# Optimization experiments

Hardware: AMD Instinct MI355X
Metric: run time of the kernel (lower is better)

The kernel has to match this reference:

```python
import jax, jax.numpy as jnp
import numpy as np

B, T, S = 4, 2048, 512
HID, ND, NH = 2048, 1024, 16
HD = HID // NH  # 128
GATING_INIT = -4.0


def setup_inputs() -> dict:
    key = jax.random.key(0)
    ks = jax.random.split(key, 12)
    sc_h = 1.0 / np.sqrt(HID)
    sc_n = 1.0 / np.sqrt(ND)
    mask = jax.random.bernoulli(ks[2], 0.9, (B, S))
    mask = mask.at[:, 0].set(True)  # avoid fully-masked rows (NaN softmax)
    return {
        "hidden_states": jax.random.normal(ks[0], (B, T, HID), jnp.float32),
        "notes": jax.random.normal(ks[1], (B, S, ND), jnp.float32),
        "notes_mask": mask,
        "q_w": jax.random.normal(ks[3], (HID, HID), jnp.float32) * sc_h,
        "q_b": jax.random.normal(ks[4], (HID,), jnp.float32) * 0.01,
        "k_w": jax.random.normal(ks[5], (HID, ND), jnp.float32) * sc_n,
        "k_b": jax.random.normal(ks[6], (HID,), jnp.float32) * 0.01,
        "v_w": jax.random.normal(ks[7], (HID, ND), jnp.float32) * sc_n,
        "v_b": jax.random.normal(ks[8], (HID,), jnp.float32) * 0.01,
        "o_w": jax.random.normal(ks[9], (HID, HID), jnp.float32) * sc_h,
        "o_b": jax.random.normal(ks[10], (HID,), jnp.float32) * 0.01,
        "gate": jnp.full((1,), GATING_INIT, jnp.float32),
    }


def reference(hidden_states, notes, notes_mask, q_w, q_b, k_w, k_b, v_w, v_b, o_w, o_b, gate):
    # projections (torch Linear: x @ W^T + b)
    q = hidden_states @ q_w.T + q_b            # (B,T,HID)
    k = notes @ k_w.T + k_b                    # (B,S,HID)
    v = notes @ v_w.T + v_b                    # (B,S,HID)
    q = q.reshape(B, T, NH, HD).transpose(0, 2, 1, 3)  # (B,H,T,D)
    k = k.reshape(B, S, NH, HD).transpose(0, 2, 1, 3)  # (B,H,S,D)
    v = v.reshape(B, S, NH, HD).transpose(0, 2, 1, 3)
    scores = jnp.einsum("bhtd,bhsd->bhts", q, k) / jnp.sqrt(jnp.float32(HD))
    scores = jnp.where(notes_mask[:, None, None, :], scores, -jnp.inf)
    attn = jax.nn.softmax(scores, axis=-1)
    context = jnp.einsum("bhts,bhsd->bhtd", attn, v)   # (B,H,T,D)
    g = jax.nn.sigmoid(gate).reshape(1, 1, 1, 1)
    context = (g * context).transpose(0, 2, 1, 3).reshape(B, T, HID)
    delta = context @ o_w.T + o_b
    return delta
```

## Files before the change

kernel.cpp:

```cpp
#include <hip/hip_runtime.h>
#include <hip/hip_bf16.h>
#include <stdint.h>

#define B_ 4
#define T_ 2048
#define S_ 512
#define HID_ 2048
#define ND_ 1024
#define NH_ 16
#define HD_ 128

typedef unsigned short u16;
typedef unsigned int u32;
typedef __attribute__((ext_vector_type(8))) short bf16x8;
typedef __attribute__((ext_vector_type(4))) float f32x4;
typedef __attribute__((ext_vector_type(16))) float f32x16;
typedef __attribute__((ext_vector_type(4))) float f4;
typedef __attribute__((ext_vector_type(4))) u16 us4;
typedef __attribute__((ext_vector_type(8))) u16 us8;
typedef __attribute__((ext_vector_type(4))) u32 u32x4;

__device__ inline u16 f2bf(float f) {
  unsigned u = __builtin_bit_cast(unsigned, f);
  u += 0x7FFFu + ((u >> 16) & 1u);
  return (u16)(u >> 16);
}

__device__ inline u32 cvtpk(float lo, float hi) {
  u32 r;
  asm("v_cvt_pk_bf16_f32 %0, %1, %2" : "=v"(r) : "v"(lo), "v"(hi));
  return r;
}

__device__ inline f32x4 mfma16(bf16x8 a, bf16x8 b, f32x4 c) {
  return __builtin_amdgcn_mfma_f32_16x16x32_bf16(a, b, c, 0, 0, 0);
}
__device__ inline f32x16 mfma32(bf16x8 a, bf16x8 b, f32x16 c) {
  return __builtin_amdgcn_mfma_f32_32x32x16_bf16(a, b, c, 0, 0, 0);
}

__device__ inline void gload_lds16(const u16* g, u16* l) {
  __builtin_amdgcn_global_load_lds(
      (const __attribute__((address_space(1))) unsigned int*)g,
      (__attribute__((address_space(3))) unsigned int*)l, 16, 0, 0);
}

__global__ __launch_bounds__(256) void convert_all(
    const float* __restrict__ h, const float* __restrict__ n,
    const float* __restrict__ qw, const float* __restrict__ kw,
    const float* __restrict__ vw, const float* __restrict__ ow,
    u16* __restrict__ dh, u16* __restrict__ dn, u16* __restrict__ dqw,
    u16* __restrict__ dkw, u16* __restrict__ dvw, u16* __restrict__ dow) {
  const int C0 = 4194304;
  const int C1 = C0 + 524288;
  const int C2 = C1 + 1048576;
  const int C3 = C2 + 524288;
  const int C4 = C3 + 524288;
  const int C5 = C4 + 1048576;
  for (int c = blockIdx.x * blockDim.x + threadIdx.x; c < C5;
       c += gridDim.x * blockDim.x) {
    const float* s; u16* d; int o;
    if (c < C0)      { s = h;  d = dh;  o = c; }
    else if (c < C1) { s = n;  d = dn;  o = c - C0; }
    else if (c < C2) { s = qw; d = dqw; o = c - C1; }
    else if (c < C3) { s = kw; d = dkw; o = c - C2; }
    else if (c < C4) { s = vw; d = dvw; o = c - C3; }
    else             { s = ow; d = dow; o = c - C4; }
    f4 v = ((const f4*)s)[o];
    us4 r = { f2bf(v[0]), f2bf(v[1]), f2bf(v[2]), f2bf(v[3]) };
    ((us4*)d)[o] = r;
  }
}

template <bool OUT_BF16>
__global__ __launch_bounds__(256) void gemm_bt(
    const u16* __restrict__ A, const u16* __restrict__ Bm,
    const float* __restrict__ bias, void* __restrict__ Cout,
    int M, int N, int K) {
  __shared__ u16 As[128 * 32];
  __shared__ u16 Bs[128 * 32];
  const int tid = threadIdx.x;
  const int lane = tid & 63;
  const int wave = tid >> 6;
  const int wr = (wave >> 1) * 64;
  const int wc = (wave & 1) * 64;
  const int c15 = lane & 15;
  const int g = lane >> 4;
  const int bx = blockIdx.x, by = blockIdx.y;

  const u16* gA = A + (size_t)(by * 128 + (tid >> 2)) * K + (tid & 3) * 8;
  const u16* gB = Bm + (size_t)(bx * 128 + (tid >> 2)) * K + (tid & 3) * 8;

  f32x4 acc[4][4];
#pragma unroll
  for (int i = 0; i < 4; ++i)
#pragma unroll
    for (int j = 0; j < 4; ++j) acc[i][j] = (f32x4){0.f, 0.f, 0.f, 0.f};

  for (int k0 = 0; k0 < K; k0 += 32) {
    gload_lds16(gA + k0, &As[wave * 512]);
    gload_lds16(gA + (size_t)64 * K + k0, &As[2048 + wave * 512]);
    gload_lds16(gB + k0, &Bs[wave * 512]);
    gload_lds16(gB + (size_t)64 * K + k0, &Bs[2048 + wave * 512]);
    __syncthreads();
    bf16x8 af[4], bfr[4];
#pragma unroll
    for (int mt = 0; mt < 4; ++mt)
      af[mt] = *(const bf16x8*)&As[(wr + mt * 16 + c15) * 32 + g * 8];
#pragma unroll
    for (int nt = 0; nt < 4; ++nt)
      bfr[nt] = *(const bf16x8*)&Bs[(wc + nt * 16 + c15) * 32 + g * 8];
#pragma unroll
    for (int mt = 0; mt < 4; ++mt)
#pragma unroll
      for (int nt = 0; nt < 4; ++nt)
        acc[mt][nt] = mfma16(af[mt], bfr[nt], acc[mt][nt]);
    __syncthreads();
  }

#pragma unroll
  for (int mt = 0; mt < 4; ++mt)
#pragma unroll
    for (int nt = 0; nt < 4; ++nt) {
      const int m = by * 128 + wr + mt * 16 + g * 4;
      const int n = bx * 128 + wc + nt * 16 + c15;
      const float bv = bias[n];
#pragma unroll
      for (int r = 0; r < 4; ++r) {
        const float v = acc[mt][nt][r] + bv;
        if (OUT_BF16)
          ((u16*)Cout)[(size_t)(m + r) * N + n] = f2bf(v);
        else
          ((float*)Cout)[(size_t)(m + r) * N + n] = v;
      }
    }
}

template <bool OUT_BF16>
__global__ __launch_bounds__(512, 2) void gemm256(
    const u16* __restrict__ A, const u16* __restrict__ Bm,
    const float* __restrict__ bias, void* __restrict__ Cout,
    int M, int N, int K) {
  extern __shared__ u16 lds[];
  const int tid = threadIdx.x;
  const int lane = tid & 63, wave = tid >> 6;
  const int wm = wave >> 2, wn = wave & 3;
  const int c15 = lane & 15, g = lane >> 4;
  const int bid = blockIdx.y * gridDim.x + blockIdx.x;
  const int sw = (bid & 7) * 32 + (bid >> 3);
  const int bn = sw & 7, bm = sw >> 3;
  const int NT = K >> 5;

  const int srow = tid >> 2;
  const int sx = (tid & 3) ^ ((srow >> 1) & 3);
  const u16* pa0 = A + (size_t)(bm * 256 + srow) * K + sx * 8;
  const u16* pa1 = A + (size_t)(bm * 256 + 128 + srow) * K + sx * 8;
  const u16* pb0 = Bm + (size_t)(bn * 256 + srow) * K + sx * 8;
  const u16* pb1 = Bm + (size_t)(bn * 256 + 128 + srow) * K + sx * 8;

  const int xr = (c15 >> 1) & 3;
  const int aoff = wm * 4096 + c15 * 32 + ((g ^ xr)) * 8;
  const int boff = 8192 + wn * 2048 + c15 * 32 + ((g ^ xr)) * 8;

  f32x4 acc[8][4];
#pragma unroll
  for (int i = 0; i < 8; ++i)
#pragma unroll
    for (int j = 0; j < 4; ++j) acc[i][j] = (f32x4){0.f, 0.f, 0.f, 0.f};

  {
    u16* sA = lds + wave * 512;
    u16* sB = lds + 8192 + wave * 512;
    gload_lds16(pa0, sA);          gload_lds16(pa1, sA + 4096);
    gload_lds16(pb0, sB);          gload_lds16(pb1, sB + 4096);
    pa0 += 32; pa1 += 32; pb0 += 32; pb1 += 32;
    gload_lds16(pa0, sA + 16384);  gload_lds16(pa1, sA + 20480);
    gload_lds16(pb0, sB + 16384);  gload_lds16(pb1, sB + 20480);
    pa0 += 32; pa1 += 32; pb0 += 32; pb1 += 32;
  }
  asm volatile("s_waitcnt vmcnt(4)" ::: "memory");
  __builtin_amdgcn_s_barrier();
  __builtin_amdgcn_sched_barrier(0);

  int curo = 0, stgo = 32768;
  for (int t = 0; t < NT; ++t) {
    const bool more = (t + 2 < NT);
    const u16* cb = lds + curo;
    bf16x8 a[4], b[4];
#pragma unroll
    for (int mf = 0; mf < 4; ++mf)
      a[mf] = *(const bf16x8*)(cb + aoff + mf * 512);
#pragma unroll
    for (int nf = 0; nf < 4; ++nf)
      b[nf] = *(const bf16x8*)(cb + boff + nf * 512);
    if (more) {
      gload_lds16(pa0, lds + stgo + wave * 512);
      gload_lds16(pa1, lds + stgo + 4096 + wave * 512);
    }
    __builtin_amdgcn_s_barrier();
    __builtin_amdgcn_sched_barrier(0);
    __builtin_amdgcn_s_setprio(1);
#pragma unroll
    for (int mf = 0; mf < 4; ++mf)
#pragma unroll
      for (int nf = 0; nf < 4; ++nf)
        acc[mf][nf] = mfma16(a[mf], b[nf], acc[mf][nf]);
    __builtin_amdgcn_s_setprio(0);
    __builtin_amdgcn_s_barrier();
    __builtin_amdgcn_sched_barrier(0);
    bf16x8 a2[4];
#pragma unroll
    for (int mf = 0; mf < 4; ++mf)
      a2[mf] = *(const bf16x8*)(cb + aoff + (4 + mf) * 512);
    if (more) {
      gload_lds16(pb0, lds + stgo + 8192 + wave * 512);
      gload_lds16(pb1, lds + stgo + 12288 + wave * 512);
      pa0 += 32; pa1 += 32; pb0 += 32; pb1 += 32;
    }
    __builtin_amdgcn_s_barrier();
    __builtin_amdgcn_sched_barrier(0);
    __builtin_amdgcn_s_setprio(1);
#pragma unroll
    for (int mf = 0; mf < 4; ++mf)
#pragma unroll
      for (int nf = 0; nf < 4; ++nf)
        acc[4 + mf][nf] = mfma16(a2[mf], b[nf], acc[4 + mf][nf]);
    __builtin_amdgcn_s_setprio(0);
    if (t < NT - 1) {
      if (more) asm volatile("s_waitcnt vmcnt(4)" ::: "memory");
      else      asm volatile("s_waitcnt vmcnt(0)" ::: "memory");
    }
    __builtin_amdgcn_s_barrier();
    __builtin_amdgcn_sched_barrier(0);
    curo = (curo == 32768) ? 0 : curo + 16384;
    stgo = (stgo == 32768) ? 0 : stgo + 16384;
  }

#pragma unroll
  for (int mf = 0; mf < 8; ++mf)
#pragma unroll
    for (int nf = 0; nf < 4; ++nf) {
      const int m = bm * 256 + wm * 128 + mf * 16 + g * 4;
      const int n = bn * 256 + wn * 64 + nf * 16 + c15;
      const float bv = bias[n];
#pragma unroll
      for (int r = 0; r < 4; ++r) {
        const float v = acc[mf][nf][r] + bv;
        if (OUT_BF16)
          ((u16*)Cout)[(size_t)(m + r) * N + n] = f2bf(v);
        else
          ((float*)Cout)[(size_t)(m + r) * N + n] = v;
      }
    }
}

__global__ __launch_bounds__(256) void transpose_v(const u16* __restrict__ v,
                                                   u16* __restrict__ vt) {
  __shared__ u16 tile[32][36];
  const int s0 = blockIdx.x * 32;
  const int bh = blockIdx.y;
  const int d0 = blockIdx.z * 32;
  const int b = bh >> 4, h = bh & 15;
  const int tid = threadIdx.x;
  const int sl = tid >> 3, dl = (tid & 7) * 4;
  us4 val = *(const us4*)(v + (size_t)(b * S_ + s0 + sl) * HID_ + h * HD_ + d0 + dl);
  *(us4*)&tile[sl][dl] = val;
  __syncthreads();
  const int dl2 = tid >> 3, sl2 = (tid & 7) * 4;
  us4 outv = { tile[sl2 + 0][dl2], tile[sl2 + 1][dl2],
               tile[sl2 + 2][dl2], tile[sl2 + 3][dl2] };
  *(us4*)(vt + ((size_t)bh * HD_ + d0 + dl2) * S_ + s0 + sl2) = outv;
}

__global__ __launch_bounds__(256) void attn_fwd(
    const u16* __restrict__ q, const u16* __restrict__ k,
    const u16* __restrict__ vt, const int* __restrict__ mask,
    const float* __restrict__ gate, u16* __restrict__ ctx) {
  __shared__ u16 smem[17408];
  __shared__ float addend[S_];
  const int tid = threadIdx.x, lane = tid & 63, wave = tid >> 6;
  const int bh = blockIdx.y, b = bh >> 4, h = bh & 15;
  const int tw = blockIdx.x * 128 + wave * 32;
  const int l31 = lane & 31, hi = lane >> 5;

  const u16* kb  = k + (size_t)b * S_ * HID_ + h * HD_;
  const u16* vtb = vt + (size_t)bh * HD_ * S_;

  const u16* sp[4];
  int dj[4];
  u16* ldsbase;
  ptrdiff_t stride;
  if (wave < 2) {
    ldsbase = smem;
    stride = 32 * HID_;
#pragma unroll
    for (int i = 0; i < 4; ++i) {
      const int jj = wave * 4 + i;
      const int row = jj * 4 + (lane >> 4);
      const int cb = (lane & 15) * 16;
      const int cbp = cb ^ ((row & 7) << 4);
      sp[i] = kb + (size_t)row * HID_ + (cbp >> 1);
      dj[i] = jj * 512;
    }
  } else {
    ldsbase = smem + 8192;
    stride = 32;
#pragma unroll
    for (int i = 0; i < 4; ++i) {
      const int jj = (wave - 2) * 4 + i;
      const int d = jj * 16 + (lane >> 2);
      const int cb = (lane & 3) * 16;
      const int cbp = cb ^ ((d & 3) << 4);
      sp[i] = vtb + (size_t)d * S_ + (cbp >> 1);
      dj[i] = jj * 512;
    }
  }
#define STAGE(cur)                                            \
  do {                                                        \
    _Pragma("unroll") for (int i_ = 0; i_ < 4; ++i_) {        \
      gload_lds16(sp[i_], ldsbase + (cur) * 4096 + dj[i_]);   \
      sp[i_] += stride;                                       \
    }                                                         \
  } while (0)

  STAGE(0);

  for (int s = tid; s < S_; s += 256)
    addend[s] = mask[b * S_ + s] ? 0.f : -1e30f;

  const u16* qrow = q + (size_t)(b * T_ + tw + l31) * HID_ + h * HD_;
  bf16x8 qf[8];
#pragma unroll
  for (int dc = 0; dc < 8; ++dc)
    qf[dc] = *(const bf16x8*)&qrow[dc * 16 + hi * 8];

  int kofs[8];
#pragma unroll
  for (int dc = 0; dc < 8; ++dc)
    kofs[dc] = l31 * 128 + (((dc * 32 + hi * 16) ^ ((l31 & 7) << 4)) >> 1);
  const int vcol0 = ((hi * 16) ^ ((l31 & 3) << 4)) >> 1;
  const int vcol1 = ((32 + hi * 16) ^ ((l31 & 3) << 4)) >> 1;

  float m_run = -1e30f, l_run = 0.f;
  f32x16 ct[4];
#pragma unroll
  for (int i = 0; i < 4; ++i)
#pragma unroll
    for (int r = 0; r < 16; ++r) ct[i][r] = 0.f;
  const float scale = 0.08838834764831845f;

  __syncthreads();

  for (int it = 0; it < 16; ++it) {
    const int cur = it & 1;
    if (it < 15) STAGE(cur ^ 1);
    const int s0 = it * 32;
    const u16* kt = smem + cur * 4096;
    const u16* vl = smem + 8192 + cur * 4096;

    f32x16 st;
#pragma unroll
    for (int r = 0; r < 16; ++r) st[r] = 0.f;
    __builtin_amdgcn_s_setprio(1);
#pragma unroll
    for (int dc = 0; dc < 8; ++dc) {
      bf16x8 kf = *(const bf16x8*)&kt[kofs[dc]];
      st = mfma32(kf, qf[dc], st);
    }
    __builtin_amdgcn_s_setprio(0);

    float sc[16];
#pragma unroll
    for (int rq = 0; rq < 4; ++rq) {
      f4 ad = *(const f4*)&addend[s0 + rq * 8 + hi * 4];
#pragma unroll
      for (int m = 0; m < 4; ++m)
        sc[rq * 4 + m] = st[rq * 4 + m] * scale + ad[m];
    }
    float tm = sc[0];
#pragma unroll
    for (int i = 1; i < 16; ++i) tm = fmaxf(tm, sc[i]);
    tm = fmaxf(tm, __shfl_xor(tm, 32));
    const float nm = fmaxf(m_run, tm);
    if (!__all(nm - m_run <= 8.f)) {
      const float corr = __expf(m_run - nm);
      l_run *= corr;
#pragma unroll
      for (int db = 0; db < 4; ++db)
#pragma unroll
        for (int r = 0; r < 16; ++r) ct[db][r] *= corr;
      m_run = nm;
    }
    float p[16], ps = 0.f;
#pragma unroll
    for (int i = 0; i < 16; ++i) { p[i] = __expf(sc[i] - m_run); ps += p[i]; }
    ps += __shfl_xor(ps, 32);
    l_run += ps;

    u32 w[8], x[8];
#pragma unroll
    for (int q2 = 0; q2 < 4; ++q2) {
      w[2 * q2]     = cvtpk(p[4 * q2],     p[4 * q2 + 1]);
      w[2 * q2 + 1] = cvtpk(p[4 * q2 + 2], p[4 * q2 + 3]);
    }
#pragma unroll
    for (int i = 0; i < 8; ++i) x[i] = __shfl_xor((int)w[i], 32);
    const u32x4 f0 = hi ? (u32x4){x[2], x[3], w[2], w[3]}
                        : (u32x4){w[0], w[1], x[0], x[1]};
    const u32x4 f1 = hi ? (u32x4){x[6], x[7], w[6], w[7]}
                        : (u32x4){w[4], w[5], x[4], x[5]};
    const bf16x8 pf0 = __builtin_bit_cast(bf16x8, f0);
    const bf16x8 pf1 = __builtin_bit_cast(bf16x8, f1);

    __builtin_amdgcn_s_setprio(1);
#pragma unroll
    for (int db = 0; db < 4; ++db) {
      bf16x8 vf0 = *(const bf16x8*)&vl[db * 1024 + l31 * 32 + vcol0];
      ct[db] = mfma32(vf0, pf0, ct[db]);
      bf16x8 vf1 = *(const bf16x8*)&vl[db * 1024 + l31 * 32 + vcol1];
      ct[db] = mfma32(vf1, pf1, ct[db]);
    }
    __builtin_amdgcn_s_setprio(0);

    __syncthreads();
  }
#undef STAGE

  const float gsig = 1.f / (1.f + __expf(-gate[0]));
  const float inv = gsig / l_run;
  u16* c_lds = smem + wave * 4352;
#pragma unroll
  for (int db = 0; db < 4; ++db)
#pragma unroll
    for (int rq = 0; rq < 4; ++rq) {
      us4 o = { f2bf(ct[db][rq * 4 + 0] * inv), f2bf(ct[db][rq * 4 + 1] * inv),
                f2bf(ct[db][rq * 4 + 2] * inv), f2bf(ct[db][rq * 4 + 3] * inv) };
      *(us4*)&c_lds[l31 * 136 + db * 32 + rq * 8 + hi * 4] = o;
    }
  u16* crow = ctx + (size_t)(b * T_ + tw) * HID_ + h * HD_;
#pragma unroll
  for (int rep = 0; rep < 8; ++rep) {
    const int tt = (lane >> 4) + rep * 4;
    us8 valv = *(const us8*)&c_lds[tt * 136 + (lane & 15) * 8];
    *(us8*)&crow[(size_t)tt * HID_ + (lane & 15) * 8] = valv;
  }
}

extern "C" void kernel_launch(void* const* d_in, const int* in_sizes, int n_in,
                              void* d_out, int out_size, void* d_ws, size_t ws_size,
                              hipStream_t stream) {
  (void)in_sizes; (void)n_in; (void)out_size; (void)ws_size;
  const float* hs   = (const float*)d_in[0];
  const float* nts  = (const float*)d_in[1];
  const int*   mask = (const int*)d_in[2];
  const float* qw   = (const float*)d_in[3];
  const float* qb   = (const float*)d_in[4];
  const float* kw   = (const float*)d_in[5];
  const float* kbi  = (const float*)d_in[6];
  const float* vw   = (const float*)d_in[7];
  const float* vbi  = (const float*)d_in[8];
  const float* ow   = (const float*)d_in[9];
  const float* obi  = (const float*)d_in[10];
  const float* gate = (const float*)d_in[11];
  float* out = (float*)d_out;

  char* w = (char*)d_ws;
  u16* h_bf   = (u16*)(w + 0);
  u16* n_bf   = (u16*)(w + 33554432);
  u16* qw_bf  = (u16*)(w + 37748736);
  u16* kw_bf  = (u16*)(w + 46137344);
  u16* vw_bf  = (u16*)(w + 50331648);
  u16* ow_bf  = (u16*)(w + 54525952);
  u16* q_bf   = (u16*)(w + 62914560);
  u16* k_bf   = (u16*)(w + 96468992);
  u16* v_bf   = (u16*)(w + 104857600);
  u16* vt_bf  = (u16*)(w + 113246208);
  u16* ctx_bf = h_bf;

  hipFuncSetAttribute(reinterpret_cast<const void*>(&gemm256<true>),
                      hipFuncAttributeMaxDynamicSharedMemorySize, 98304);
  hipFuncSetAttribute(reinterpret_cast<const void*>(&gemm256<false>),
                      hipFuncAttributeMaxDynamicSharedMemorySize, 98304);

  convert_all<<<dim3(2048), dim3(256), 0, stream>>>(
      hs, nts, qw, kw, vw, ow, h_bf, n_bf, qw_bf, kw_bf, vw_bf, ow_bf);
  gemm_bt<true><<<dim3(16, 16), dim3(256), 0, stream>>>(
      n_bf, kw_bf, kbi, k_bf, 2048, 2048, 1024);
  gemm_bt<true><<<dim3(16, 16), dim3(256), 0, stream>>>(
      n_bf, vw_bf, vbi, v_bf, 2048, 2048, 1024);
  transpose_v<<<dim3(16, 64, 4), dim3(256), 0, stream>>>(v_bf, vt_bf);
  gemm256<true><<<dim3(8, 32), dim3(512), 98304, stream>>>(
      h_bf, qw_bf, qb, q_bf, 8192, 2048, 2048);
  attn_fwd<<<dim3(16, 64), dim3(256), 0, stream>>>(
      q_bf, k_bf, vt_bf, mask, gate, ctx_bf);
  gemm256<false><<<dim3(8, 32), dim3(512), 98304, stream>>>(
      ctx_bf, ow_bf, obi, out, 8192, 2048, 2048);
}
```

Baseline: 285.7 us.

## Retile large GEMMs to 256x128 blocks with 4 waves per workgroup

The Q and output projection GEMMs change from 256x256 tiles with 8 waves to 256x128 tiles with 4 waves. The grid doubles to 512 blocks and LDS per block drops to 72KB, and each wave now issues more global-to-LDS loads to cover the tile. The aim is better CU fill and occupancy across the 256 CUs. The cost is lower B-operand reuse per block, since A is read twice as often overall.

New measurement: 291.4 us. About the same (+2.0%).

```diff
diff --git a/kernel.cpp b/kernel.cpp
--- a/kernel.cpp
+++ b/kernel.cpp
@@ -137,30 +137,39 @@
 }
 
 template <bool OUT_BF16>
-__global__ __launch_bounds__(512, 2) void gemm256(
+__global__ __launch_bounds__(256, 2) void gemm_big(
     const u16* __restrict__ A, const u16* __restrict__ Bm,
     const float* __restrict__ bias, void* __restrict__ Cout,
     int M, int N, int K) {
   extern __shared__ u16 lds[];
   const int tid = threadIdx.x;
   const int lane = tid & 63, wave = tid >> 6;
-  const int wm = wave >> 2, wn = wave & 3;
+  const int wm = wave >> 1, wn = wave & 1;
   const int c15 = lane & 15, g = lane >> 4;
   const int bid = blockIdx.y * gridDim.x + blockIdx.x;
-  const int sw = (bid & 7) * 32 + (bid >> 3);
-  const int bn = sw & 7, bm = sw >> 3;
+  const int sw = (bid & 7) * 64 + (bid >> 3);
+  const int bn = sw & 15, bm = sw >> 4;
   const int NT = K >> 5;
 
-  const int srow = tid >> 2;
-  const int sx = (tid & 3) ^ ((srow >> 1) & 3);
-  const u16* pa0 = A + (size_t)(bm * 256 + srow) * K + sx * 8;
-  const u16* pa1 = A + (size_t)(bm * 256 + 128 + srow) * K + sx * 8;
-  const u16* pb0 = Bm + (size_t)(bn * 256 + srow) * K + sx * 8;
-  const u16* pb1 = Bm + (size_t)(bn * 256 + 128 + srow) * K + sx * 8;
+  const int rsub = lane >> 2, chunk = lane & 3;
+  const u16* pA[4]; const u16* pB[2];
+  int dA[4], dB[2];
+#pragma unroll
+  for (int i = 0; i < 4; ++i) {
+    const int rg = (i * 4 + wave) * 16 + rsub;
+    pA[i] = A + (size_t)(bm * 256 + rg) * K + (chunk ^ ((rg >> 1) & 3)) * 8;
+    dA[i] = (i * 4 + wave) * 512;
+  }
+#pragma unroll
+  for (int j = 0; j < 2; ++j) {
+    const int rg = (j * 4 + wave) * 16 + rsub;
+    pB[j] = Bm + (size_t)(bn * 128 + rg) * K + (chunk ^ ((rg >> 1) & 3)) * 8;
+    dB[j] = 8192 + (j * 4 + wave) * 512;
+  }
 
   const int xr = (c15 >> 1) & 3;
-  const int aoff = wm * 4096 + c15 * 32 + ((g ^ xr)) * 8;
-  const int boff = 8192 + wn * 2048 + c15 * 32 + ((g ^ xr)) * 8;
+  const int aoff = (wm * 128 + c15) * 32 + (g ^ xr) * 8;
+  const int boff = 8192 + (wn * 64 + c15) * 32 + (g ^ xr) * 8;
 
   f32x4 acc[8][4];
 #pragma unroll
@@ -168,21 +177,27 @@
 #pragma unroll
     for (int j = 0; j < 4; ++j) acc[i][j] = (f32x4){0.f, 0.f, 0.f, 0.f};
 
-  {
-    u16* sA = lds + wave * 512;
-    u16* sB = lds + 8192 + wave * 512;
-    gload_lds16(pa0, sA);          gload_lds16(pa1, sA + 4096);
-    gload_lds16(pb0, sB);          gload_lds16(pb1, sB + 4096);
-    pa0 += 32; pa1 += 32; pb0 += 32; pb1 += 32;
-    gload_lds16(pa0, sA + 16384);  gload_lds16(pa1, sA + 20480);
-    gload_lds16(pb0, sB + 16384);  gload_lds16(pb1, sB + 20480);
-    pa0 += 32; pa1 += 32; pb0 += 32; pb1 += 32;
-  }
-  asm volatile("s_waitcnt vmcnt(4)" ::: "memory");
+#pragma unroll
+  for (int i = 0; i < 4; ++i) gload_lds16(pA[i], lds + dA[i]);
+#pragma unroll
+  for (int j = 0; j < 2; ++j) gload_lds16(pB[j], lds + dB[j]);
+#pragma unroll
+  for (int i = 0; i < 4; ++i) pA[i] += 32;
+#pragma unroll
+  for (int j = 0; j < 2; ++j) pB[j] += 32;
+#pragma unroll
+  for (int i = 0; i < 4; ++i) gload_lds16(pA[i], lds + 12288 + dA[i]);
+#pragma unroll
+  for (int j = 0; j < 2; ++j) gload_lds16(pB[j], lds + 12288 + dB[j]);
+#pragma unroll
+  for (int i = 0; i < 4; ++i) pA[i] += 32;
+#pragma unroll
+  for (int j = 0; j < 2; ++j) pB[j] += 32;
+  asm volatile("s_waitcnt vmcnt(6)" ::: "memory");
   __builtin_amdgcn_s_barrier();
   __builtin_amdgcn_sched_barrier(0);
 
-  int curo = 0, stgo = 32768;
+  int curo = 0, stgo = 24576;
   for (int t = 0; t < NT; ++t) {
     const bool more = (t + 2 < NT);
     const u16* cb = lds + curo;
@@ -194,8 +209,8 @@
     for (int nf = 0; nf < 4; ++nf)
       b[nf] = *(const bf16x8*)(cb + boff + nf * 512);
     if (more) {
-      gload_lds16(pa0, lds + stgo + wave * 512);
-      gload_lds16(pa1, lds + stgo + 4096 + wave * 512);
+#pragma unroll
+      for (int i = 0; i < 4; ++i) gload_lds16(pA[i], lds + stgo + dA[i]);
     }
     __builtin_amdgcn_s_barrier();
     __builtin_amdgcn_sched_barrier(0);
@@ -213,9 +228,12 @@
     for (int mf = 0; mf < 4; ++mf)
       a2[mf] = *(const bf16x8*)(cb + aoff + (4 + mf) * 512);
     if (more) {
-      gload_lds16(pb0, lds + stgo + 8192 + wave * 512);
-      gload_lds16(pb1, lds + stgo + 12288 + wave * 512);
-      pa0 += 32; pa1 += 32; pb0 += 32; pb1 += 32;
+#pragma unroll
+      for (int j = 0; j < 2; ++j) gload_lds16(pB[j], lds + stgo + dB[j]);
+#pragma unroll
+      for (int i = 0; i < 4; ++i) pA[i] += 32;
+#pragma unroll
+      for (int j = 0; j < 2; ++j) pB[j] += 32;
     }
     __builtin_amdgcn_s_barrier();
     __builtin_amdgcn_sched_barrier(0);
@@ -227,13 +245,13 @@
         acc[4 + mf][nf] = mfma16(a2[mf], b[nf], acc[4 + mf][nf]);
     __builtin_amdgcn_s_setprio(0);
     if (t < NT - 1) {
-      if (more) asm volatile("s_waitcnt vmcnt(4)" ::: "memory");
+      if (more) asm volatile("s_waitcnt vmcnt(6)" ::: "memory");
       else      asm volatile("s_waitcnt vmcnt(0)" ::: "memory");
     }
     __builtin_amdgcn_s_barrier();
     __builtin_amdgcn_sched_barrier(0);
-    curo = (curo == 32768) ? 0 : curo + 16384;
-    stgo = (stgo == 32768) ? 0 : stgo + 16384;
+    curo = (curo == 24576) ? 0 : curo + 12288;
+    stgo = (stgo == 24576) ? 0 : stgo + 12288;
   }
 
 #pragma unroll
@@ -241,7 +259,7 @@
 #pragma unroll
     for (int nf = 0; nf < 4; ++nf) {
       const int m = bm * 256 + wm * 128 + mf * 16 + g * 4;
-      const int n = bn * 256 + wn * 64 + nf * 16 + c15;
+      const int n = bn * 128 + wn * 64 + nf * 16 + c15;
       const float bv = bias[n];
 #pragma unroll
       for (int r = 0; r < 4; ++r) {
@@ -477,10 +495,10 @@
   u16* vt_bf  = (u16*)(w + 113246208);
   u16* ctx_bf = h_bf;
 
-  hipFuncSetAttribute(reinterpret_cast<const void*>(&gemm256<true>),
-                      hipFuncAttributeMaxDynamicSharedMemorySize, 98304);
-  hipFuncSetAttribute(reinterpret_cast<const void*>(&gemm256<false>),
-                      hipFuncAttributeMaxDynamicSharedMemorySize, 98304);
+  hipFuncSetAttribute(reinterpret_cast<const void*>(&gemm_big<true>),
+                      hipFuncAttributeMaxDynamicSharedMemorySize, 73728);
+  hipFuncSetAttribute(reinterpret_cast<const void*>(&gemm_big<false>),
+                      hipFuncAttributeMaxDynamicSharedMemorySize, 73728);
 
   convert_all<<<dim3(2048), dim3(256), 0, stream>>>(
       hs, nts, qw, kw, vw, ow, h_bf, n_bf, qw_bf, kw_bf, vw_bf, ow_bf);
@@ -489,10 +507,10 @@
   gemm_bt<true><<<dim3(16, 16), dim3(256), 0, stream>>>(
       n_bf, vw_bf, vbi, v_bf, 2048, 2048, 1024);
   transpose_v<<<dim3(16, 64, 4), dim3(256), 0, stream>>>(v_bf, vt_bf);
-  gemm256<true><<<dim3(8, 32), dim3(512), 98304, stream>>>(
+  gemm_big<true><<<dim3(16, 32), dim3(256), 73728, stream>>>(
       h_bf, qw_bf, qb, q_bf, 8192, 2048, 2048);
   attn_fwd<<<dim3(16, 64), dim3(256), 0, stream>>>(
       q_bf, k_bf, vt_bf, mask, gate, ctx_bf);
-  gemm256<false><<<dim3(8, 32), dim3(512), 98304, stream>>>(
+  gemm_big<false><<<dim3(16, 32), dim3(256), 73728, stream>>>(
       ctx_bf, ow_bf, obi, out, 8192, 2048, 2048);
 }
```

## Use four-stage LDS ring in GEMM with one barrier per K-step

Applied to the files above, without the earlier changes.

The 256x256 GEMM's LDS buffering moves from a three-slot rotating scheme to a four-slot ring indexed by t&3, with a prefetch distance of two K-steps. Each iteration now reads all A and B fragments up front, issues all four global-to-LDS loads at once, runs all 32 MFMAs in one block, then waits and hits a single barrier. The previous version split the step into two halves separated by three barriers. This is meant to cut barrier and scheduling overhead and give loads longer to land, at the cost of 128KB of dynamic LDS and holding more fragment registers live.

Result: no change. 280.8 us (-1.7%).

```diff
diff --git a/kernel.cpp b/kernel.cpp
--- a/kernel.cpp
+++ b/kernel.cpp
@@ -137,7 +137,7 @@
 }
 
 template <bool OUT_BF16>
-__global__ __launch_bounds__(512, 2) void gemm256(
+__global__ __launch_bounds__(512, 2) void gemm_pipe(
     const u16* __restrict__ A, const u16* __restrict__ Bm,
     const float* __restrict__ bias, void* __restrict__ Cout,
     int M, int N, int K) {
@@ -159,8 +159,8 @@
   const u16* pb1 = Bm + (size_t)(bn * 256 + 128 + srow) * K + sx * 8;
 
   const int xr = (c15 >> 1) & 3;
-  const int aoff = wm * 4096 + c15 * 32 + ((g ^ xr)) * 8;
-  const int boff = 8192 + wn * 2048 + c15 * 32 + ((g ^ xr)) * 8;
+  const int aoff = wm * 4096 + c15 * 32 + (g ^ xr) * 8;
+  const int boff = 8192 + wn * 2048 + c15 * 32 + (g ^ xr) * 8;
 
   f32x4 acc[8][4];
 #pragma unroll
@@ -180,60 +180,42 @@
   }
   asm volatile("s_waitcnt vmcnt(4)" ::: "memory");
   __builtin_amdgcn_s_barrier();
-  __builtin_amdgcn_sched_barrier(0);
-
-  int curo = 0, stgo = 32768;
+
   for (int t = 0; t < NT; ++t) {
     const bool more = (t + 2 < NT);
-    const u16* cb = lds + curo;
-    bf16x8 a[4], b[4];
+    const u16* cb = lds + (t & 3) * 16384;
+    u16* sb = lds + ((t + 2) & 3) * 16384;
+
+    bf16x8 a[8], b[4];
 #pragma unroll
     for (int mf = 0; mf < 4; ++mf)
       a[mf] = *(const bf16x8*)(cb + aoff + mf * 512);
 #pragma unroll
     for (int nf = 0; nf < 4; ++nf)
       b[nf] = *(const bf16x8*)(cb + boff + nf * 512);
+#pragma unroll
+    for (int mf = 4; mf < 8; ++mf)
+      a[mf] = *(const bf16x8*)(cb + aoff + mf * 512);
+
     if (more) {
-      gload_lds16(pa0, lds + stgo + wave * 512);
-      gload_lds16(pa1, lds + stgo + 4096 + wave * 512);
-    }
-    __builtin_amdgcn_s_barrier();
-    __builtin_amdgcn_sched_barrier(0);
+      gload_lds16(pa0, sb + wave * 512);
+      gload_lds16(pa1, sb + 4096 + wave * 512);
+      gload_lds16(pb0, sb + 8192 + wave * 512);
+      gload_lds16(pb1, sb + 12288 + wave * 512);
+      pa0 += 32; pa1 += 32; pb0 += 32; pb1 += 32;
+    }
+
     __builtin_amdgcn_s_setprio(1);
 #pragma unroll
-    for (int mf = 0; mf < 4; ++mf)
+    for (int mf = 0; mf < 8; ++mf)
 #pragma unroll
       for (int nf = 0; nf < 4; ++nf)
         acc[mf][nf] = mfma16(a[mf], b[nf], acc[mf][nf]);
     __builtin_amdgcn_s_setprio(0);
+
+    if (more) asm volatile("s_waitcnt vmcnt(4)" ::: "memory");
+    else      asm volatile("s_waitcnt vmcnt(0)" ::: "memory");
     __builtin_amdgcn_s_barrier();
-    __builtin_amdgcn_sched_barrier(0);
-    bf16x8 a2[4];
-#pragma unroll
-    for (int mf = 0; mf < 4; ++mf)
-      a2[mf] = *(const bf16x8*)(cb + aoff + (4 + mf) * 512);
-    if (more) {
-      gload_lds16(pb0, lds + stgo + 8192 + wave * 512);
-      gload_lds16(pb1, lds + stgo + 12288 + wave * 512);
-      pa0 += 32; pa1 += 32; pb0 += 32; pb1 += 32;
-    }
-    __builtin_amdgcn_s_barrier();
-    __builtin_amdgcn_sched_barrier(0);
-    __builtin_amdgcn_s_setprio(1);
-#pragma unroll
-    for (int mf = 0; mf < 4; ++mf)
-#pragma unroll
-      for (int nf = 0; nf < 4; ++nf)
-        acc[4 + mf][nf] = mfma16(a2[mf], b[nf], acc[4 + mf][nf]);
-    __builtin_amdgcn_s_setprio(0);
-    if (t < NT - 1) {
-      if (more) asm volatile("s_waitcnt vmcnt(4)" ::: "memory");
-      else      asm volatile("s_waitcnt vmcnt(0)" ::: "memory");
-    }
-    __builtin_amdgcn_s_barrier();
-    __builtin_amdgcn_sched_barrier(0);
-    curo = (curo == 32768) ? 0 : curo + 16384;
-    stgo = (stgo == 32768) ? 0 : stgo + 16384;
   }
 
 #pragma unroll
@@ -477,10 +459,10 @@
   u16* vt_bf  = (u16*)(w + 113246208);
   u16* ctx_bf = h_bf;
 
-  hipFuncSetAttribute(reinterpret_cast<const void*>(&gemm256<true>),
-                      hipFuncAttributeMaxDynamicSharedMemorySize, 98304);
-  hipFuncSetAttribute(reinterpret_cast<const void*>(&gemm256<false>),
-                      hipFuncAttributeMaxDynamicSharedMemorySize, 98304);
+  hipFuncSetAttribute(reinterpret_cast<const void*>(&gemm_pipe<true>),
+                      hipFuncAttributeMaxDynamicSharedMemorySize, 131072);
+  hipFuncSetAttribute(reinterpret_cast<const void*>(&gemm_pipe<false>),
+                      hipFuncAttributeMaxDynamicSharedMemorySize, 131072);
 
   convert_all<<<dim3(2048), dim3(256), 0, stream>>>(
       hs, nts, qw, kw, vw, ow, h_bf, n_bf, qw_bf, kw_bf, vw_bf, ow_bf);
@@ -489,10 +471,10 @@
   gemm_bt<true><<<dim3(16, 16), dim3(256), 0, stream>>>(
       n_bf, vw_bf, vbi, v_bf, 2048, 2048, 1024);
   transpose_v<<<dim3(16, 64, 4), dim3(256), 0, stream>>>(v_bf, vt_bf);
-  gemm256<true><<<dim3(8, 32), dim3(512), 98304, stream>>>(
+  gemm_pipe<true><<<dim3(8, 32), dim3(512), 131072, stream>>>(
       h_bf, qw_bf, qb, q_bf, 8192, 2048, 2048);
   attn_fwd<<<dim3(16, 64), dim3(256), 0, stream>>>(
       q_bf, k_bf, vt_bf, mask, gate, ctx_bf);
-  gemm256<false><<<dim3(8, 32), dim3(512), 98304, stream>>>(
+  gemm_pipe<false><<<dim3(8, 32), dim3(512), 131072, stream>>>(
       ctx_bf, ow_bf, obi, out, 8192, 2048, 2048);
 }
```
